# Optimization experiments

Measured on AMD Instinct MI355X. Metric: run time of the kernel, lower is better.

## Reference

```python
import jax, jax.numpy as jnp
import numpy as np

B, T, C = 4, 2048, 768   # batch, seq, n_embd
E, K = 8, 2              # n_routed_experts, moe_top_k (expert hidden dim == C per source)


def setup_inputs() -> dict:
    key = jax.random.key(0)
    ks = jax.random.split(key, 6)
    s = 0.02  # init scale to keep relu(x)^2 well-behaved
    return {
        "x": jax.random.normal(ks[0], (B, T, C), jnp.float32),
        "w_fc_sh": jax.random.normal(ks[1], (C, C), jnp.float32) * s,    # shared expert c_fc (stored [in,out])
        "w_proj_sh": jax.random.normal(ks[2], (C, C), jnp.float32) * s,  # shared expert c_proj
        "w1": jax.random.normal(ks[3], (E, C, C), jnp.float32) * s,      # routed experts c_fc, [E,in,out]
        "w2": jax.random.normal(ks[4], (E, C, C), jnp.float32) * s,      # routed experts c_proj
        "router_w": jax.random.normal(ks[5], (E, C), jnp.float32) * s,   # router weight [E, C]
        "balance_bias": jnp.zeros((E,), jnp.float32),                    # router balance_bias buffer
    }


def _mlp(x, wfc, wproj):
    # MLP: c_proj(relu(c_fc(x))**2)
    h = jnp.square(jax.nn.relu(x @ wfc))
    return h @ wproj


def reference(x, w_fc_sh, w_proj_sh, w1, w2, router_w, balance_bias):
    Bx, Tx, Cx = x.shape
    shared = _mlp(x, w_fc_sh, w_proj_sh)                    # [B,T,C]

    xf = x.reshape(-1, Cx)                                  # [N,C]
    # --- router ---
    logits = xf.astype(jnp.float32) @ router_w.T            # [N,E]
    scores = jax.nn.sigmoid(logits)
    _, idx = jax.lax.top_k(scores + balance_bias, K)        # selection uses biased scores
    tw = jnp.take_along_axis(scores, idx, axis=-1)          # gate weights from unbiased scores
    tw = tw / (tw.sum(-1, keepdims=True) + 1e-20)           # [N,K]

    # per-token per-expert combine weights (equivalent to gather/MLP/index_add loop)
    combine = (jax.nn.one_hot(idx, E, dtype=tw.dtype) * tw[..., None]).sum(1)  # [N,E]

    # dense all-expert compute, masked combine (same math as sparse dispatch)
    h = jnp.square(jax.nn.relu(jnp.einsum('nc,ech->neh', xf, w1)))  # [N,E,H]
    y = jnp.einsum('neh,ehc->nec', h, w2)                            # [N,E,C]
    routed = jnp.einsum('nec,ne->nc', y, combine)                    # [N,C]

    return shared + routed.reshape(Bx, Tx, Cx)
```

## Files before the change

### kernel.cpp

```cpp
#include <hip/hip_runtime.h>
#include <stdint.h>

#define N_TOK 8192
#define C_DIM 768
#define E_NUM 8
#define NTK 24
#define GRIDG 624
#define PREP_WT 10368
#define PREP_TOT (PREP_WT + N_TOK / 4)

typedef short short8 __attribute__((ext_vector_type(8)));
typedef __bf16 bf16x8 __attribute__((ext_vector_type(8)));
typedef float f32x4 __attribute__((ext_vector_type(4)));

static __device__ __forceinline__ unsigned short f2bf(float f) {
    unsigned u = __float_as_uint(f);
    unsigned r = u + 0x7FFFu + ((u >> 16) & 1u);
    return (unsigned short)(r >> 16);
}
static __device__ __forceinline__ float bf2f(unsigned short h) {
    return __uint_as_float(((unsigned)h) << 16);
}

__global__ __launch_bounds__(256) void prep_kernel(const float* __restrict__ wfc,
                                                   const float* __restrict__ wpj,
                                                   const float* __restrict__ w1,
                                                   const float* __restrict__ w2,
                                                   unsigned short* __restrict__ Wt,
                                                   const float* __restrict__ x,
                                                   const float* __restrict__ rw,
                                                   const float* __restrict__ bias,
                                                   float* __restrict__ topk_w,
                                                   int* __restrict__ eids,
                                                   unsigned short* __restrict__ xb) {
    __shared__ float tile[32][33];
    const int bx = blockIdx.x;
    const int t = threadIdx.x;
    if (bx < PREP_WT) {
        const int m = bx / 576;
        const int rem = bx - m * 576;
        const int i0 = (rem / 24) * 32;
        const int o0 = (rem % 24) * 32;
        const int tx = t & 31, ty = t >> 5;
        const float* src = (m == 0) ? wfc : (m == 1) ? wpj
                         : (m < 10) ? (w1 + (size_t)(m - 2) * C_DIM * C_DIM)
                                    : (w2 + (size_t)(m - 10) * C_DIM * C_DIM);
        #pragma unroll
        for (int rr = 0; rr < 32; rr += 8)
            tile[ty + rr][tx] = src[(size_t)(i0 + ty + rr) * C_DIM + o0 + tx];
        __syncthreads();
        unsigned short* dst = Wt + (size_t)m * C_DIM * C_DIM;
        #pragma unroll
        for (int rr = 0; rr < 32; rr += 8) {
            int o = o0 + ty + rr;
            dst[(size_t)o * C_DIM + i0 + tx] = f2bf(tile[tx][ty + rr]);
        }
    } else {
        const int rb = bx - PREP_WT;
        const int wave = t >> 6;
        const int lane = t & 63;
        const int n = rb * 4 + wave;
        const float* xp = x + (size_t)n * C_DIM + lane * 12;
        float xv[12];
        #pragma unroll
        for (int j = 0; j < 12; j++) xv[j] = xp[j];
        unsigned short* xbp = xb + (size_t)n * C_DIM + lane * 12;
        #pragma unroll
        for (int j = 0; j < 12; j++) xbp[j] = f2bf(xv[j]);
        float acc[E_NUM];
        #pragma unroll
        for (int e = 0; e < E_NUM; e++) acc[e] = 0.f;
        #pragma unroll
        for (int e = 0; e < E_NUM; e++) {
            const float* wp = rw + (size_t)e * C_DIM + lane * 12;
            #pragma unroll
            for (int j = 0; j < 12; j++) acc[e] += xv[j] * wp[j];
        }
        #pragma unroll
        for (int e = 0; e < E_NUM; e++) {
            #pragma unroll
            for (int off = 32; off > 0; off >>= 1) acc[e] += __shfl_xor(acc[e], off, 64);
        }
        if (lane == 0) {
            float sc[E_NUM];
            #pragma unroll
            for (int e = 0; e < E_NUM; e++) sc[e] = 1.f / (1.f + expf(-acc[e]));
            int e0 = 0; float best = -1e30f;
            #pragma unroll
            for (int e = 0; e < E_NUM; e++) { float v = sc[e] + bias[e]; if (v > best) { best = v; e0 = e; } }
            int e1 = -1; float best1 = -1e30f;
            #pragma unroll
            for (int e = 0; e < E_NUM; e++) { if (e == e0) continue; float v = sc[e] + bias[e]; if (v > best1) { best1 = v; e1 = e; } }
            float w0 = sc[e0], w1 = sc[e1];
            float s = w0 + w1 + 1e-20f;
            w0 /= s; w1 /= s;
            topk_w[n * 2] = w0; topk_w[n * 2 + 1] = w1;
            eids[n * 2] = e0; eids[n * 2 + 1] = e1;
        }
    }
}

__global__ __launch_bounds__(1024) void bucketize_kernel(const int* __restrict__ eids,
                                                         int* __restrict__ counts,
                                                         int* __restrict__ buckets) {
    const int e = blockIdx.x;
    const int t = threadIdx.x;
    const int wv = t >> 6, lane = t & 63;
    __shared__ int wave_tot[16];
    int running = 0;
    for (int start = 0; start < 2 * N_TOK; start += 1024) {
        const int i = start + t;
        const int f = (eids[i] == e) ? 1 : 0;
        unsigned long long mask = __ballot(f);
        int pre = __popcll(mask & ((1ull << lane) - 1ull));
        if (lane == 0) wave_tot[wv] = __popcll(mask);
        __syncthreads();
        int wbase = 0, tot = 0;
        #pragma unroll
        for (int j = 0; j < 16; j++) { int c = wave_tot[j]; tot += c; if (j < wv) wbase += c; }
        if (f) buckets[e * N_TOK + running + wbase + pre] = i;
        running += tot;
        __syncthreads();
    }
    if (t == 0) counts[e] = running;
}

#define GLOAD_LDS(g, l) __builtin_amdgcn_global_load_lds((const __attribute__((address_space(1))) void*)(g), (__attribute__((address_space(3))) void*)(l), 16, 0, 0)
#define WAITVM0() asm volatile("s_waitcnt vmcnt(0)" ::: "memory")
#define SCHEDB() __builtin_amdgcn_sched_barrier(0)
#define BAR() __builtin_amdgcn_s_barrier()

template <int PHASE>
__global__ __launch_bounds__(512, 4) void gemm_all_kernel(const unsigned short* __restrict__ Adir,
                                                          const unsigned short* __restrict__ Agat,
                                                          const unsigned short* __restrict__ WtAll,
                                                          void* __restrict__ dstDir,
                                                          unsigned short* __restrict__ dstGat,
                                                          const int* __restrict__ counts,
                                                          const int* __restrict__ buckets) {
    const int fid = blockIdx.x;
    const int xcd = fid & 7;
    const int i6 = fid >> 3;
    const int xx = xcd + 8 * (i6 / 6);
    const int y = i6 % 6;
    int cz[E_NUM];
    #pragma unroll
    for (int zz = 0; zz < E_NUM; zz++) cz[zz] = counts[zz];
    int xo[E_NUM + 1]; int a = 0;
    #pragma unroll
    for (int zz = 0; zz < E_NUM; zz++) { xo[zz] = a; a += (cz[zz] + 255) >> 8; }
    xo[E_NUM] = a;
    if (xx >= a + 32) return;
    const bool sh = (xx >= a);
    int z = 0, xl = xx - a;
    if (!sh) {
        #pragma unroll
        for (int zz = 0; zz < E_NUM; zz++)
            if (xx >= xo[zz] && xx < xo[zz + 1]) { z = zz; xl = xx - xo[zz]; }
    }
    const int rows = sh ? N_TOK : cz[z];
    const int r0 = xl * 256;
    const int c0 = y * 128;

    __shared__ __align__(16) unsigned short lds[2 * 12288];

    const int t = threadIdx.x;
    const int lane = t & 63;
    const int wv = t >> 6;
    const int wm = wv >> 1;
    const int wn = wv & 1;

    const int widx = sh ? (PHASE == 0 ? 0 : 1) : (PHASE == 0 ? 2 + z : 10 + z);
    const unsigned short* Bmat = WtAll + (size_t)widx * C_DIM * C_DIM;
    const int* bk = buckets + z * N_TOK;

    const int scol = (((lane & 3) ^ ((lane >> 3) & 3)) * 8);
    const int rA0 = wv * 16 + (lane >> 2);
    const int rA1 = 128 + rA0;
    int g0, g1;
    const unsigned short* Asrc;
    if (sh) {
        Asrc = Adir;
        g0 = r0 + rA0; g1 = r0 + rA1;
    } else {
        Asrc = Agat;
        int p0 = r0 + rA0, p1 = r0 + rA1;
        int e0v = bk[p0 < rows ? p0 : rows - 1];
        int e1v = bk[p1 < rows ? p1 : rows - 1];
        g0 = (PHASE == 0) ? (e0v >> 1) : e0v;
        g1 = (PHASE == 0) ? (e1v >> 1) : e1v;
    }
    const unsigned short* ap0 = Asrc + (size_t)g0 * C_DIM + scol;
    const unsigned short* ap1 = Asrc + (size_t)g1 * C_DIM + scol;
    const unsigned short* bp  = Bmat + (size_t)(c0 + rA0) * C_DIM + scol;

    f32x4 acc[4][4];
    #pragma unroll
    for (int i = 0; i < 4; i++)
        #pragma unroll
        for (int j = 0; j < 4; j++) acc[i][j] = (f32x4){0.f, 0.f, 0.f, 0.f};

    const int fr = lane & 15;
    const int fq = lane >> 4;
    const int ks = ((fq ^ ((fr >> 1) & 3)) * 8);

    GLOAD_LDS(ap0, lds + wv * 512 + lane * 8);
    GLOAD_LDS(ap1, lds + 4096 + wv * 512 + lane * 8);
    GLOAD_LDS(bp,  lds + 8192 + wv * 512 + lane * 8);

    #pragma unroll
    for (int kt = 0; kt < NTK; ++kt) {
        WAITVM0();
        BAR();
        SCHEDB();
        if (kt + 1 < NTK) {
            unsigned short* d = lds + ((kt + 1) & 1) * 12288;
            const int ko = (kt + 1) * 32;
            GLOAD_LDS(ap0 + ko, d + wv * 512 + lane * 8);
            GLOAD_LDS(ap1 + ko, d + 4096 + wv * 512 + lane * 8);
            GLOAD_LDS(bp + ko,  d + 8192 + wv * 512 + lane * 8);
        }
        SCHEDB();
        const unsigned short* buf = lds + (kt & 1) * 12288;
        short8 afr[4], bfr[4];
        #pragma unroll
        for (int i = 0; i < 4; i++)
            afr[i] = *reinterpret_cast<const short8*>(buf + (size_t)(wm * 64 + i * 16 + fr) * 32 + ks);
        #pragma unroll
        for (int j = 0; j < 4; j++)
            bfr[j] = *reinterpret_cast<const short8*>(buf + 8192 + (size_t)(wn * 64 + j * 16 + fr) * 32 + ks);
        __builtin_amdgcn_s_setprio(1);
        #pragma unroll
        for (int i = 0; i < 4; i++)
            #pragma unroll
            for (int j = 0; j < 4; j++)
                acc[i][j] = __builtin_amdgcn_mfma_f32_16x16x32_bf16(
                    __builtin_bit_cast(bf16x8, afr[i]), __builtin_bit_cast(bf16x8, bfr[j]), acc[i][j], 0, 0, 0);
        __builtin_amdgcn_s_setprio(0);
    }

    const int orow = r0 + wm * 64;
    const int ocol = c0 + wn * 64;
    if (sh) {
        if constexpr (PHASE == 0) {
            unsigned short* Hd = (unsigned short*)dstDir;
            #pragma unroll
            for (int i = 0; i < 4; i++)
                #pragma unroll
                for (int rr = 0; rr < 4; rr++) {
                    size_t base = (size_t)(orow + i * 16 + fq * 4 + rr) * C_DIM;
                    #pragma unroll
                    for (int j = 0; j < 4; j++) {
                        float v = acc[i][j][rr];
                        float rl = v > 0.f ? v : 0.f;
                        Hd[base + ocol + j * 16 + fr] = f2bf(rl * rl);
                    }
                }
        } else {
            float* od = (float*)dstDir;
            #pragma unroll
            for (int i = 0; i < 4; i++)
                #pragma unroll
                for (int rr = 0; rr < 4; rr++) {
                    size_t base = (size_t)(orow + i * 16 + fq * 4 + rr) * C_DIM;
                    #pragma unroll
                    for (int j = 0; j < 4; j++)
                        od[base + ocol + j * 16 + fr] = acc[i][j][rr];
                }
        }
    } else {
        #pragma unroll
        for (int i = 0; i < 4; i++)
            #pragma unroll
            for (int rr = 0; rr < 4; rr++) {
                int pos = orow + i * 16 + fq * 4 + rr;
                if (pos < rows) {
                    int ent = bk[pos];
                    size_t base = (size_t)ent * C_DIM;
                    #pragma unroll
                    for (int j = 0; j < 4; j++) {
                        float v = acc[i][j][rr];
                        if (PHASE == 0) {
                            float rl = v > 0.f ? v : 0.f;
                            dstGat[base + ocol + j * 16 + fr] = f2bf(rl * rl);
                        } else {
                            dstGat[base + ocol + j * 16 + fr] = f2bf(v);
                        }
                    }
                }
            }
    }
}

__global__ void combine_kernel(float* __restrict__ out, const unsigned short* __restrict__ Y,
                               const float* __restrict__ tw) {
    int idx = blockIdx.x * blockDim.x + threadIdx.x;
    const int per_row = C_DIM / 4;
    if (idx >= N_TOK * per_row) return;
    int n = idx / per_row;
    int c = (idx % per_row) * 4;
    float w0 = tw[n * 2], w1 = tw[n * 2 + 1];
    const ushort4 a = *reinterpret_cast<const ushort4*>(Y + (size_t)(n * 2) * C_DIM + c);
    const ushort4 b = *reinterpret_cast<const ushort4*>(Y + (size_t)(n * 2 + 1) * C_DIM + c);
    float4* op = reinterpret_cast<float4*>(out + (size_t)n * C_DIM + c);
    float4 o = *op;
    o.x += w0 * bf2f(a.x) + w1 * bf2f(b.x);
    o.y += w0 * bf2f(a.y) + w1 * bf2f(b.y);
    o.z += w0 * bf2f(a.z) + w1 * bf2f(b.z);
    o.w += w0 * bf2f(a.w) + w1 * bf2f(b.w);
    *op = o;
}

extern "C" void kernel_launch(void* const* d_in, const int* in_sizes, int n_in,
                              void* d_out, int out_size, void* d_ws, size_t ws_size,
                              hipStream_t stream) {
    const float* x   = (const float*)d_in[0];
    const float* wfc = (const float*)d_in[1];
    const float* wpj = (const float*)d_in[2];
    const float* w1  = (const float*)d_in[3];
    const float* w2  = (const float*)d_in[4];
    const float* rw  = (const float*)d_in[5];
    const float* bias= (const float*)d_in[6];
    float* out = (float*)d_out;

    char* ws = (char*)d_ws;
    size_t off = 0;
    auto alloc = [&](size_t bytes) { void* p = ws + off; off += (bytes + 255) & ~(size_t)255; return p; };
    unsigned short* xb   = (unsigned short*)alloc((size_t)N_TOK * C_DIM * 2);
    unsigned short* Wt   = (unsigned short*)alloc((size_t)18 * C_DIM * C_DIM * 2);
    unsigned short* H    = (unsigned short*)alloc((size_t)N_TOK * 2 * C_DIM * 2);
    unsigned short* Hsh  = (unsigned short*)alloc((size_t)N_TOK * C_DIM * 2);
    unsigned short* Y    = (unsigned short*)alloc((size_t)N_TOK * 2 * C_DIM * 2);
    float* topk_w        = (float*)alloc((size_t)N_TOK * 2 * 4);
    int* counts          = (int*)alloc(256);
    int* buckets         = (int*)alloc((size_t)E_NUM * N_TOK * 4);
    int* eids            = (int*)alloc((size_t)2 * N_TOK * 4);

    prep_kernel<<<PREP_TOT, 256, 0, stream>>>(wfc, wpj, w1, w2, Wt, x, rw, bias, topk_w, eids, xb);
    bucketize_kernel<<<E_NUM, 1024, 0, stream>>>(eids, counts, buckets);

    gemm_all_kernel<0><<<GRIDG, 512, 0, stream>>>(xb, xb, Wt, Hsh, H, counts, buckets);
    gemm_all_kernel<1><<<GRIDG, 512, 0, stream>>>(Hsh, H, Wt, out, Y, counts, buckets);

    combine_kernel<<<(N_TOK * (C_DIM / 4) + 255) / 256, 256, 0, stream>>>(out, Y, topk_w);
}
```

Baseline: 145.2 us.

## Shrink GEMM tiles to 128x128 with 4 waves and balanced per-XCD work mapping

The grouped GEMM tile shrinks from 256x128 with 8 waves to 128x128 with 4 waves, with per-expert row blocks now rounded to 128 instead of 256. Blocks map to work items through a contiguous per-XCD partition of the real work count instead of a fixed XCD-strided formula. The grid grows to 1200 and the early exit handles unused blocks. This cuts padding waste on ragged expert buckets and should improve load balance and occupancy, at the cost of fewer FLOPs per loaded byte and more blocks.

```diff
diff --git a/kernel.cpp b/kernel.cpp
--- a/kernel.cpp
+++ b/kernel.cpp
@@ -5,7 +5,7 @@
 #define C_DIM 768
 #define E_NUM 8
 #define NTK 24
-#define GRIDG 624
+#define GRIDF 1200
 #define PREP_WT 10368
 #define PREP_TOT (PREP_WT + N_TOK / 4)
 
@@ -131,26 +131,31 @@
 #define BAR() __builtin_amdgcn_s_barrier()
 
 template <int PHASE>
-__global__ __launch_bounds__(512, 4) void gemm_all_kernel(const unsigned short* __restrict__ Adir,
+__global__ __launch_bounds__(256, 5) void gemm_all_kernel(const unsigned short* __restrict__ Adir,
                                                           const unsigned short* __restrict__ Agat,
                                                           const unsigned short* __restrict__ WtAll,
                                                           void* __restrict__ dstDir,
                                                           unsigned short* __restrict__ dstGat,
                                                           const int* __restrict__ counts,
                                                           const int* __restrict__ buckets) {
-    const int fid = blockIdx.x;
-    const int xcd = fid & 7;
-    const int i6 = fid >> 3;
-    const int xx = xcd + 8 * (i6 / 6);
-    const int y = i6 % 6;
     int cz[E_NUM];
     #pragma unroll
     for (int zz = 0; zz < E_NUM; zz++) cz[zz] = counts[zz];
     int xo[E_NUM + 1]; int a = 0;
     #pragma unroll
-    for (int zz = 0; zz < E_NUM; zz++) { xo[zz] = a; a += (cz[zz] + 255) >> 8; }
+    for (int zz = 0; zz < E_NUM; zz++) { xo[zz] = a; a += (cz[zz] + 127) >> 7; }
     xo[E_NUM] = a;
-    if (xx >= a + 32) return;
+    const int nw = (a + 64) * 6;
+    const int fid = blockIdx.x;
+    const int xcd = fid & 7;
+    const int idx = fid >> 3;
+    const int q = nw >> 3, r = nw & 7;
+    const int sz = q + (xcd < r ? 1 : 0);
+    if (idx >= sz) return;
+    const int wid = xcd * q + (xcd < r ? xcd : r) + idx;
+    const int xx = wid / 6;
+    const int y = wid - xx * 6;
+
     const bool sh = (xx >= a);
     int z = 0, xl = xx - a;
     if (!sh) {
@@ -159,40 +164,41 @@
             if (xx >= xo[zz] && xx < xo[zz + 1]) { z = zz; xl = xx - xo[zz]; }
     }
     const int rows = sh ? N_TOK : cz[z];
-    const int r0 = xl * 256;
+    const int r0 = xl * 128;
     const int c0 = y * 128;
 
-    __shared__ __align__(16) unsigned short lds[2 * 12288];
+    __shared__ __align__(16) unsigned short lds[2 * 8192];
 
     const int t = threadIdx.x;
     const int lane = t & 63;
     const int wv = t >> 6;
-    const int wm = wv >> 1;
-    const int wn = wv & 1;
+    const int wr = (wv >> 1) * 64;
+    const int wc = (wv & 1) * 64;
 
     const int widx = sh ? (PHASE == 0 ? 0 : 1) : (PHASE == 0 ? 2 + z : 10 + z);
     const unsigned short* Bmat = WtAll + (size_t)widx * C_DIM * C_DIM;
     const int* bk = buckets + z * N_TOK;
 
-    const int scol = (((lane & 3) ^ ((lane >> 3) & 3)) * 8);
-    const int rA0 = wv * 16 + (lane >> 2);
-    const int rA1 = 128 + rA0;
+    const int ar0 = t >> 2;
+    const int ar1 = 64 + ar0;
+    const int acol = (((t & 3) ^ ((t >> 3) & 3)) * 8);
     int g0, g1;
     const unsigned short* Asrc;
     if (sh) {
         Asrc = Adir;
-        g0 = r0 + rA0; g1 = r0 + rA1;
+        g0 = r0 + ar0; g1 = r0 + ar1;
     } else {
         Asrc = Agat;
-        int p0 = r0 + rA0, p1 = r0 + rA1;
+        int p0 = r0 + ar0, p1 = r0 + ar1;
         int e0v = bk[p0 < rows ? p0 : rows - 1];
         int e1v = bk[p1 < rows ? p1 : rows - 1];
         g0 = (PHASE == 0) ? (e0v >> 1) : e0v;
         g1 = (PHASE == 0) ? (e1v >> 1) : e1v;
     }
-    const unsigned short* ap0 = Asrc + (size_t)g0 * C_DIM + scol;
-    const unsigned short* ap1 = Asrc + (size_t)g1 * C_DIM + scol;
-    const unsigned short* bp  = Bmat + (size_t)(c0 + rA0) * C_DIM + scol;
+    const unsigned short* ap0 = Asrc + (size_t)g0 * C_DIM + acol;
+    const unsigned short* ap1 = Asrc + (size_t)g1 * C_DIM + acol;
+    const unsigned short* bp0 = Bmat + (size_t)(c0 + ar0) * C_DIM + acol;
+    const unsigned short* bp1 = Bmat + (size_t)(c0 + ar1) * C_DIM + acol;
 
     f32x4 acc[4][4];
     #pragma unroll
@@ -200,13 +206,15 @@
         #pragma unroll
         for (int j = 0; j < 4; j++) acc[i][j] = (f32x4){0.f, 0.f, 0.f, 0.f};
 
-    const int fr = lane & 15;
-    const int fq = lane >> 4;
-    const int ks = ((fq ^ ((fr >> 1) & 3)) * 8);
-
-    GLOAD_LDS(ap0, lds + wv * 512 + lane * 8);
-    GLOAD_LDS(ap1, lds + 4096 + wv * 512 + lane * 8);
-    GLOAD_LDS(bp,  lds + 8192 + wv * 512 + lane * 8);
+    const int qr = (((lane >> 4) ^ ((lane >> 1) & 3)) * 8);
+
+    {
+        unsigned short* d = lds + t * 8;
+        GLOAD_LDS(ap0, d);
+        GLOAD_LDS(ap1, d + 2048);
+        GLOAD_LDS(bp0, d + 4096);
+        GLOAD_LDS(bp1, d + 6144);
+    }
 
     #pragma unroll
     for (int kt = 0; kt < NTK; ++kt) {
@@ -214,21 +222,22 @@
         BAR();
         SCHEDB();
         if (kt + 1 < NTK) {
-            unsigned short* d = lds + ((kt + 1) & 1) * 12288;
+            unsigned short* d = lds + ((kt + 1) & 1) * 8192 + t * 8;
             const int ko = (kt + 1) * 32;
-            GLOAD_LDS(ap0 + ko, d + wv * 512 + lane * 8);
-            GLOAD_LDS(ap1 + ko, d + 4096 + wv * 512 + lane * 8);
-            GLOAD_LDS(bp + ko,  d + 8192 + wv * 512 + lane * 8);
+            GLOAD_LDS(ap0 + ko, d);
+            GLOAD_LDS(ap1 + ko, d + 2048);
+            GLOAD_LDS(bp0 + ko, d + 4096);
+            GLOAD_LDS(bp1 + ko, d + 6144);
         }
         SCHEDB();
-        const unsigned short* buf = lds + (kt & 1) * 12288;
+        const unsigned short* buf = lds + (kt & 1) * 8192;
         short8 afr[4], bfr[4];
         #pragma unroll
         for (int i = 0; i < 4; i++)
-            afr[i] = *reinterpret_cast<const short8*>(buf + (size_t)(wm * 64 + i * 16 + fr) * 32 + ks);
+            afr[i] = *reinterpret_cast<const short8*>(buf + (size_t)(wr + i * 16 + (lane & 15)) * 32 + qr);
         #pragma unroll
         for (int j = 0; j < 4; j++)
-            bfr[j] = *reinterpret_cast<const short8*>(buf + 8192 + (size_t)(wn * 64 + j * 16 + fr) * 32 + ks);
+            bfr[j] = *reinterpret_cast<const short8*>(buf + 4096 + (size_t)(wc + j * 16 + (lane & 15)) * 32 + qr);
         __builtin_amdgcn_s_setprio(1);
         #pragma unroll
         for (int i = 0; i < 4; i++)
@@ -239,8 +248,8 @@
         __builtin_amdgcn_s_setprio(0);
     }
 
-    const int orow = r0 + wm * 64;
-    const int ocol = c0 + wn * 64;
+    const int fr = lane & 15;
+    const int fq = lane >> 4;
     if (sh) {
         if constexpr (PHASE == 0) {
             unsigned short* Hd = (unsigned short*)dstDir;
@@ -248,12 +257,12 @@
             for (int i = 0; i < 4; i++)
                 #pragma unroll
                 for (int rr = 0; rr < 4; rr++) {
-                    size_t base = (size_t)(orow + i * 16 + fq * 4 + rr) * C_DIM;
+                    size_t base = (size_t)(r0 + wr + i * 16 + fq * 4 + rr) * C_DIM;
                     #pragma unroll
                     for (int j = 0; j < 4; j++) {
                         float v = acc[i][j][rr];
                         float rl = v > 0.f ? v : 0.f;
-                        Hd[base + ocol + j * 16 + fr] = f2bf(rl * rl);
+                        Hd[base + c0 + wc + j * 16 + fr] = f2bf(rl * rl);
                     }
                 }
         } else {
@@ -262,10 +271,10 @@
             for (int i = 0; i < 4; i++)
                 #pragma unroll
                 for (int rr = 0; rr < 4; rr++) {
-                    size_t base = (size_t)(orow + i * 16 + fq * 4 + rr) * C_DIM;
+                    size_t base = (size_t)(r0 + wr + i * 16 + fq * 4 + rr) * C_DIM;
                     #pragma unroll
                     for (int j = 0; j < 4; j++)
-                        od[base + ocol + j * 16 + fr] = acc[i][j][rr];
+                        od[base + c0 + wc + j * 16 + fr] = acc[i][j][rr];
                 }
         }
     } else {
@@ -273,7 +282,7 @@
         for (int i = 0; i < 4; i++)
             #pragma unroll
             for (int rr = 0; rr < 4; rr++) {
-                int pos = orow + i * 16 + fq * 4 + rr;
+                int pos = r0 + wr + i * 16 + fq * 4 + rr;
                 if (pos < rows) {
                     int ent = bk[pos];
                     size_t base = (size_t)ent * C_DIM;
@@ -282,9 +291,9 @@
                         float v = acc[i][j][rr];
                         if (PHASE == 0) {
                             float rl = v > 0.f ? v : 0.f;
-                            dstGat[base + ocol + j * 16 + fr] = f2bf(rl * rl);
+                            dstGat[base + c0 + wc + j * 16 + fr] = f2bf(rl * rl);
                         } else {
-                            dstGat[base + ocol + j * 16 + fr] = f2bf(v);
+                            dstGat[base + c0 + wc + j * 16 + fr] = f2bf(v);
                         }
                     }
                 }
@@ -339,8 +348,8 @@
     prep_kernel<<<PREP_TOT, 256, 0, stream>>>(wfc, wpj, w1, w2, Wt, x, rw, bias, topk_w, eids, xb);
     bucketize_kernel<<<E_NUM, 1024, 0, stream>>>(eids, counts, buckets);
 
-    gemm_all_kernel<0><<<GRIDG, 512, 0, stream>>>(xb, xb, Wt, Hsh, H, counts, buckets);
-    gemm_all_kernel<1><<<GRIDG, 512, 0, stream>>>(Hsh, H, Wt, out, Y, counts, buckets);
+    gemm_all_kernel<0><<<GRIDF, 256, 0, stream>>>(xb, xb, Wt, Hsh, H, counts, buckets);
+    gemm_all_kernel<1><<<GRIDF, 256, 0, stream>>>(Hsh, H, Wt, out, Y, counts, buckets);
 
     combine_kernel<<<(N_TOK * (C_DIM / 4) + 255) / 256, 256, 0, stream>>>(out, Y, topk_w);
 }
```

New measurement: 389.5 us. 2.68x slower.
